# Kernel tuning notes

Measured on AMD Instinct MI355X. Metric: run time of the kernel, lower is better.

## Reference

```python
import jax, jax.numpy as jnp
import numpy as np

# channel indices (consistent with INPUT_CHANNELS=6)
WALL, SRC_REAL, SRC_IMAG, GATE_REAL, GATE_IMAG = 0, 1, 2, 3, 4
READOUT_THRESHOLD = 0.35
EPS = 1e-08


def _neighbor_sum(a):
    # zero-padded 4-neighbor shift-sum over last two dims of [B,1,H,W]
    H, W = a.shape[-2], a.shape[-1]
    p = jnp.pad(a, ((0, 0), (0, 0), (1, 1), (1, 1)))
    return (p[:, :, 0:H, 1:W + 1] + p[:, :, 2:H + 2, 1:W + 1]
            + p[:, :, 1:H + 1, 0:W] + p[:, :, 1:H + 1, 2:W + 2])


def _phase_vectors(phase_classes):
    k = jnp.arange(phase_classes, dtype=jnp.float32)
    th = 2.0 * jnp.pi * k / phase_classes
    return jnp.stack([jnp.cos(th), jnp.sin(th)], axis=1)  # [P,2]


def _fixed_logits(vec, phase_classes):
    phases = _phase_vectors(phase_classes)
    mag2 = jnp.sum(vec ** 2, axis=1)
    none = (READOUT_THRESHOLD * READOUT_THRESHOLD - mag2) * 8.0
    phase_logits = (vec @ phases.T - READOUT_THRESHOLD) * 12.0
    return jnp.concatenate([none[:, None], phase_logits], axis=1)


def setup_inputs() -> dict:
    key = jax.random.key(0)
    k1, k2 = jax.random.split(key)
    x = jax.random.uniform(k1, (32, 6, 256, 256), dtype=jnp.float32)
    target = jax.random.randint(k2, (32, 2), 0, 256, dtype=jnp.int64 if jax.config.jax_enable_x64 else jnp.int32)
    return {"x": x, "target": target, "steps": 24}


def reference(x, target, steps):
    phase_classes = 8
    free = 1.0 - x[:, WALL:WALL + 1]
    gate_r = x[:, GATE_REAL:GATE_REAL + 1]
    gate_i = x[:, GATE_IMAG:GATE_IMAG + 1]
    wallf = (x[:, WALL:WALL + 1] > 0.5).astype(x.dtype)

    real = x[:, SRC_REAL:SRC_REAL + 1] * free
    imag = x[:, SRC_IMAG:SRC_IMAG + 1] * free
    written = (real ** 2 + imag ** 2) > EPS
    state_r, state_i = real, imag

    def step(carry, _):
        real, imag, sr, si, written = carry
        inc_r = _neighbor_sum(real)
        inc_i = _neighbor_sum(imag)
        # FIXED_PRISMION: complex multiply with gate
        nr = inc_r * gate_r - inc_i * gate_i
        ni = inc_r * gate_i + inc_i * gate_r
        pre_wall = jnp.mean(jnp.sqrt(nr * nr + ni * ni) * wallf)
        real = nr * free
        imag = ni * free
        active = ((real ** 2 + imag ** 2) > EPS) & (~written)
        sr = jnp.where(active, real, sr)
        si = jnp.where(active, imag, si)
        written = written | active
        real = jnp.where(active, real, jnp.zeros_like(real))
        imag = jnp.where(active, imag, jnp.zeros_like(imag))
        act = jnp.mean(jnp.abs(real) + jnp.abs(imag))
        return (real, imag, sr, si, written), (pre_wall, act)

    (real, imag, state_r, state_i, written), (pre_walls, acts) = jax.lax.scan(
        step, (real, imag, state_r, state_i, written), None, length=int(steps))

    vec_map = jnp.concatenate([state_r, state_i], axis=1)  # [B,2,H,W]
    wall = x[:, WALL:WALL + 1] > 0.5
    leak = jnp.mean((((jnp.sum(vec_map ** 2, axis=1, keepdims=True) ** 0.5) > 0.5) & wall).astype(x.dtype))
    pre_wall_mean = jnp.mean(pre_walls)
    act_mean = jnp.mean(acts)

    b = jnp.arange(vec_map.shape[0])
    vec = vec_map[b, :, target[:, 0], target[:, 1]]  # [B,2]
    logits = _fixed_logits(vec, phase_classes)
    return logits, leak, pre_wall_mean, act_mean
```

## Files before the change

kernel.cpp:

```cpp
#include <hip/hip_runtime.h>
#include <stdint.h>

#define EPSV 1e-8f
#define HH 256
#define WW 256
#define NB 32
#define STEPS 24
#define PLANE (HH * WW)
#define NCELL (NB * PLANE)
#define NBLK 2048
#define TBLK 512
#define CAP 8192
#define FIXS 68719476736.0


__device__ __forceinline__ float block_fsum(float v, float* sm) {
  #pragma unroll
  for (int o = 32; o; o >>= 1) v += __shfl_down(v, o, 64);
  if ((threadIdx.x & 63) == 0) sm[threadIdx.x >> 6] = v;
  __syncthreads();
  float r = 0.0f;
  if (threadIdx.x == 0) r = ((sm[0] + sm[1]) + sm[2]) + sm[3];
  __syncthreads();
  return r;
}

__device__ __forceinline__ int block_isum(int v, int* sm) {
  #pragma unroll
  for (int o = 32; o; o >>= 1) v += __shfl_down(v, o, 64);
  if ((threadIdx.x & 63) == 0) sm[threadIdx.x >> 6] = v;
  __syncthreads();
  int r = 0;
  if (threadIdx.x == 0) r = sm[0] + sm[1] + sm[2] + sm[3];
  __syncthreads();
  return r;
}

__device__ __forceinline__ int block_any(int v, int* sm) {
  if (threadIdx.x == 0) sm[0] = 0;
  __syncthreads();
  if (v) sm[0] = 1;
  __syncthreads();
  int r = sm[0];
  __syncthreads();
  return r;
}

__global__ __launch_bounds__(128) void zero_kernel(int* __restrict__ ctrl) {
  ctrl[threadIdx.x] = 0;
}

__device__ __forceinline__ float2 init_val(const float* xw, const float* xsr,
                                           const float* xsi, int y, int xc) {
  if (y < 0 || y >= HH || xc < 0 || xc >= WW) return make_float2(0.f, 0.f);
  const int yx = y * WW + xc;
  float fr = 1.0f - xw[yx];
  return make_float2(__fmul_rn(xsr[yx], fr), __fmul_rn(xsi[yx], fr));
}

__global__ __launch_bounds__(256) void fused0_kernel(
    const float* __restrict__ x, const int* __restrict__ target,
    float2* __restrict__ bufB, uint32_t* __restrict__ wrw,
    float* __restrict__ pw_part, float* __restrict__ act_part,
    int* __restrict__ ileak_part, float* __restrict__ vec,
    int* __restrict__ ctrl, int* __restrict__ list, uint32_t* __restrict__ cbm) {
  __shared__ float smf[4];
  __shared__ int smi[4];
  const int tx = threadIdx.x;
  const int blk = blockIdx.x;
  const int b = blk >> 6;
  const int y0 = (blk & 63) << 2;
  const int cbase = b * PLANE;
  const float* xw  = x + (size_t)b * 6 * PLANE;
  const float* xsr = xw + 1 * PLANE;
  const float* xsi = xw + 2 * PLANE;
  const float* xgr = xw + 3 * PLANE;
  const float* xgi = xw + 4 * PLANE;
  const int t0 = target[b * 2], t1 = target[b * 2 + 1];

  if (tx < 32) cbm[blk * 32 + tx] = 0;

  float pw = 0.0f, act = 0.0f;
  int leak = 0, any_act = 0;

  float2 rm = init_val(xw, xsr, xsi, y0 - 1, tx);
  float wallc = xw[y0 * WW + tx];
  float2 rc;
  {
    float fr = 1.0f - wallc;
    rc = make_float2(__fmul_rn(xsr[y0 * WW + tx], fr), __fmul_rn(xsi[y0 * WW + tx], fr));
  }

  #pragma unroll
  for (int k = 0; k < 4; ++k) {
    const int y = y0 + k, yx = y * WW + tx;
    float wallp = 0.0f;
    float2 rp = make_float2(0.f, 0.f);
    if (y + 1 < HH) {
      wallp = xw[yx + WW];
      float fr = 1.0f - wallp;
      rp = make_float2(__fmul_rn(xsr[yx + WW], fr), __fmul_rn(xsi[yx + WW], fr));
    }
    float2 lf = init_val(xw, xsr, xsi, y, tx - 1);
    float2 rg = init_val(xw, xsr, xsi, y, tx + 1);

    float inc_r = (rm.x + rp.x) + (lf.x + rg.x);
    float inc_i = (rm.y + rp.y) + (lf.y + rg.y);
    float gr = xgr[yx], gi = xgi[yx];
    float fr = 1.0f - wallc;

    float nr = inc_r * gr - inc_i * gi;
    float ni = inc_r * gi + inc_i * gr;
    if (wallc > 0.5f) pw += sqrtf(nr * nr + ni * ni);

    float r = __fmul_rn(nr, fr);
    float i = __fmul_rn(ni, fr);
    float mag0 = __fadd_rn(__fmul_rn(r, r), __fmul_rn(i, i));
    float magI = __fadd_rn(__fmul_rn(rc.x, rc.x), __fmul_rn(rc.y, rc.y));
    bool writtenI = magI > EPSV;
    bool active = (mag0 > EPSV) && !writtenI;

    if (magI > 0.25f && wallc > 0.5f) ++leak;
    if (active && mag0 > 0.25f && wallc > 0.5f) ++leak;

    float outr = active ? r : 0.0f;
    float outi = active ? i : 0.0f;
    bufB[cbase + yx] = make_float2(outr, outi);
    act += fabsf(outr) + fabsf(outi);
    if (active) any_act = 1;

    if (y == t0 && tx == t1) {
      vec[2 * b] = active ? r : rc.x;
      vec[2 * b + 1] = active ? i : rc.y;
    }

    unsigned long long bw = __ballot(writtenI || active);
    if ((tx & 63) == 0) {
      uint2 v; v.x = (uint32_t)bw; v.y = (uint32_t)(bw >> 32);
      *(uint2*)&wrw[(cbase + yx) >> 5] = v;
    }

    unsigned long long ba = __ballot(active);
    if (ba) {
      const int lane = tx & 63;
      const int ldr = __ffsll((unsigned long long)ba) - 1;
      unsigned lbase = 0;
      if (lane == ldr)
        lbase = atomicAdd((unsigned*)&ctrl[51], (unsigned)__popcll(ba));
      lbase = (unsigned)__shfl((int)lbase, ldr, 64);
      if (active) {
        unsigned pos = lbase + (unsigned)__popcll(ba & ((1ull << lane) - 1ull));
        if (pos < CAP) list[pos] = cbase + yx;
      }
    }
    rm = rc; rc = rp; wallc = wallp;
  }

  float pws = block_fsum(pw, smf);
  float acs = block_fsum(act, smf);
  int lks = block_isum(leak, smi);
  if (tx == 0) { pw_part[blk] = pws; act_part[blk] = acs; ileak_part[blk] = lks; }
  if (block_any(any_act, smi) && tx == 0) ctrl[1] = 1;
}

__global__ __launch_bounds__(512) void sparse1_kernel(
    const float* __restrict__ x, const int* __restrict__ target,
    const float2* __restrict__ bufB, float2* __restrict__ bufA,
    uint32_t* __restrict__ wrw, const int* __restrict__ list,
    uint32_t* __restrict__ cbm, int* __restrict__ ctrl,
    float* __restrict__ vec) {
  __shared__ long long smp[512];
  const int t = threadIdx.x;
  const int gsz = gridDim.x * 512;
  const int n0 = ctrl[51];
  if (n0 > CAP) {
    if (blockIdx.x == 0 && t == 0) ctrl[50] = 1;
    return;
  }
  if (n0 == 0) return;

  long long pwf = 0, actf = 0;
  int leak = 0;

  for (int idx = blockIdx.x * 512 + t; idx < 5 * n0; idx += gsz) {
    const int i = idx / 5, d = idx - 5 * i;
    int cell = list[i];
    int yx = cell & 0xFFFF;
    int y = yx >> 8, xx = yx & 255;
    if (d == 1) { if (y == 0) continue;      cell -= WW; y -= 1; }
    else if (d == 2) { if (y == HH - 1) continue; cell += WW; y += 1; }
    else if (d == 3) { if (xx == 0) continue;     cell -= 1;  xx -= 1; }
    else if (d == 4) { if (xx == WW - 1) continue; cell += 1; xx += 1; }
    const uint32_t bit = 1u << (cell & 31);
    if (atomicOr(&cbm[cell >> 5], bit) & bit) continue;

    const int b = cell >> 16;
    yx = cell & 0xFFFF;
    const float* xw = x + (size_t)b * 6 * PLANE;
    float2 up = (y > 0)       ? bufB[cell - WW] : make_float2(0.f, 0.f);
    float2 dn = (y < HH - 1)  ? bufB[cell + WW] : make_float2(0.f, 0.f);
    float2 lf = (xx > 0)      ? bufB[cell - 1]  : make_float2(0.f, 0.f);
    float2 rg = (xx < WW - 1) ? bufB[cell + 1]  : make_float2(0.f, 0.f);
    float inc_r = (up.x + dn.x) + (lf.x + rg.x);
    float inc_i = (up.y + dn.y) + (lf.y + rg.y);
    float gr = xw[3 * PLANE + yx], gi = xw[4 * PLANE + yx];
    float wall = xw[yx];
    float fr = 1.0f - wall;
    float nr = inc_r * gr - inc_i * gi;
    float ni = inc_r * gi + inc_i * gr;
    if (wall > 0.5f) pwf += (long long)((double)sqrtf(nr * nr + ni * ni) * FIXS);
    float r = __fmul_rn(nr, fr);
    float i2 = __fmul_rn(ni, fr);
    float mag = __fadd_rn(__fmul_rn(r, r), __fmul_rn(i2, i2));
    bool wr = (wrw[cell >> 5] >> (cell & 31)) & 1u;
    bool active = (mag > EPSV) && !wr;
    float outr = active ? r : 0.0f;
    float outi = active ? i2 : 0.0f;
    bufA[cell] = make_float2(outr, outi);
    actf += (long long)((double)(fabsf(outr) + fabsf(outi)) * FIXS);
    if (active) {
      atomicOr(&wrw[cell >> 5], bit);
      ctrl[2] = 1;
      if (mag > 0.25f && wall > 0.5f) ++leak;
      if (y == target[b * 2] && xx == target[b * 2 + 1]) {
        vec[2 * b] = r; vec[2 * b + 1] = i2;
      }
    }
  }

  smp[t] = pwf; __syncthreads();
  for (int o = 256; o; o >>= 1) { if (t < o) smp[t] += smp[t + o]; __syncthreads(); }
  if (t == 0 && smp[0]) atomicAdd((unsigned long long*)&ctrl[56], (unsigned long long)smp[0]);
  __syncthreads();
  smp[t] = actf; __syncthreads();
  for (int o = 256; o; o >>= 1) { if (t < o) smp[t] += smp[t + o]; __syncthreads(); }
  if (t == 0 && smp[0]) atomicAdd((unsigned long long*)&ctrl[58], (unsigned long long)smp[0]);
  __syncthreads();
  smp[t] = leak; __syncthreads();
  for (int o = 256; o; o >>= 1) { if (t < o) smp[t] += smp[t + o]; __syncthreads(); }
  if (t == 0 && smp[0]) atomicAdd(&ctrl[52], (int)smp[0]);
}

__device__ __forceinline__ void grid_barrier(int* bar) {
  __syncthreads();
  if (threadIdx.x == 0) {
    __threadfence();
    __hip_atomic_fetch_add(bar, 1, __ATOMIC_RELEASE, __HIP_MEMORY_SCOPE_AGENT);
    int guard = 0;
    while (__hip_atomic_load(bar, __ATOMIC_ACQUIRE, __HIP_MEMORY_SCOPE_AGENT) < TBLK) {
      if (++guard > (1 << 22)) break;
    }
  }
  __syncthreads();
}

__global__ __launch_bounds__(256, 2) void tail_kernel(
    const float* __restrict__ x, const int* __restrict__ target,
    float2* __restrict__ bufA, float2* __restrict__ bufB,
    const uint32_t* __restrict__ wrw, const uint32_t* __restrict__ cbm,
    float* __restrict__ pw_part, float* __restrict__ act_part,
    int* __restrict__ ileak_part, float* __restrict__ vec,
    int* __restrict__ ctrl) {
  int* cnt = ctrl;
  int* bar = ctrl + 25;
  const int ov = ctrl[50];
  const int sstart = ov ? 1 : 2;
  if (cnt[sstart] == 0) return;
  __shared__ float smf[4];
  __shared__ int smi[4];
  const int tx = threadIdx.x;
  const int blk = blockIdx.x;
  const int b = blk >> 4;
  const int y0 = (blk & 15) << 4;
  const int cbase = b * PLANE;
  const float* xw  = x + (size_t)b * 6 * PLANE;
  const float* xgr = xw + 3 * PLANE;
  const float* xgi = xw + 4 * PLANE;
  const int t0 = target[b * 2], t1 = target[b * 2 + 1];

  float wallr[16];
  unsigned wrmask = 0;
  #pragma unroll
  for (int k = 0; k < 16; ++k) {
    const int yx = (y0 + k) * WW + tx;
    wallr[k] = xw[yx];
    if ((wrw[(cbase + yx) >> 5] >> (tx & 31)) & 1u) wrmask |= (1u << k);
  }

  if (!ov) {
    #pragma unroll
    for (int k = 0; k < 16; ++k) {
      const int c = cbase + (y0 + k) * WW + tx;
      if (!((cbm[c >> 5] >> (c & 31)) & 1u)) bufA[c] = make_float2(0.f, 0.f);
    }
    grid_barrier(&bar[0]);
  }

  const float2* cur0 = ov ? (const float2*)bufB : (const float2*)bufA;
  float2* nxt0 = ov ? bufA : bufB;

  for (int s = sstart; s < STEPS; ++s) {
    if (__hip_atomic_load(&cnt[s], __ATOMIC_RELAXED, __HIP_MEMORY_SCOPE_AGENT) == 0) break;
    const int p = (s - sstart) & 1;
    const float2* __restrict__ cur = p ? (const float2*)nxt0 : cur0;
    float2* __restrict__ nxt = p ? (float2*)cur0 : nxt0;

    float pw = 0.0f, act = 0.0f;
    int leak_s = 0, any_act = 0;

    float2 rowm = (y0 > 0) ? cur[cbase + (y0 - 1) * WW + tx] : make_float2(0.f, 0.f);
    float2 rowc = cur[cbase + y0 * WW + tx];

    #pragma unroll
    for (int k = 0; k < 16; ++k) {
      const int y = y0 + k, yx = y * WW + tx;
      float2 rowp = (y < HH - 1) ? cur[cbase + yx + WW] : make_float2(0.f, 0.f);
      float2 lft  = (tx > 0)      ? cur[cbase + yx - 1] : make_float2(0.f, 0.f);
      float2 rgt  = (tx < WW - 1) ? cur[cbase + yx + 1] : make_float2(0.f, 0.f);

      float inc_r = (rowm.x + rowp.x) + (lft.x + rgt.x);
      float inc_i = (rowm.y + rowp.y) + (lft.y + rgt.y);
      float gr = xgr[yx], gi = xgi[yx];
      float wall = wallr[k];
      float fr = 1.0f - wall;

      float nr = inc_r * gr - inc_i * gi;
      float ni = inc_r * gi + inc_i * gr;
      if (wall > 0.5f) pw += sqrtf(nr * nr + ni * ni);

      float r = __fmul_rn(nr, fr);
      float i = __fmul_rn(ni, fr);
      float mag = __fadd_rn(__fmul_rn(r, r), __fmul_rn(i, i));
      bool active = (mag > EPSV) && !((wrmask >> k) & 1u);

      float outr = active ? r : 0.0f;
      float outi = active ? i : 0.0f;
      nxt[cbase + yx] = make_float2(outr, outi);
      act += fabsf(outr) + fabsf(outi);

      if (active) {
        wrmask |= (1u << k);
        any_act = 1;
        if (mag > 0.25f && wall > 0.5f) ++leak_s;
        if (y == t0 && tx == t1) { vec[2 * b] = r; vec[2 * b + 1] = i; }
      }
      rowm = rowc; rowc = rowp;
    }

    float pws = block_fsum(pw, smf);
    float acs = block_fsum(act, smf);
    int lks = block_isum(leak_s, smi);
    if (tx == 0) {
      pw_part[s * NBLK + blk] = pws;
      act_part[s * NBLK + blk] = acs;
      ileak_part[s * NBLK + blk] = lks;
    }
    if (block_any(any_act, smi) && tx == 0)
      __hip_atomic_store(&cnt[s + 1], 1, __ATOMIC_RELAXED, __HIP_MEMORY_SCOPE_AGENT);
    grid_barrier(&bar[s]);
  }
}

__global__ __launch_bounds__(256) void final_kernel(
    const float* __restrict__ pw_part, const float* __restrict__ act_part,
    const int* __restrict__ ileak_part, const int* __restrict__ ctrl,
    const float* __restrict__ vec, float* __restrict__ out) {
  __shared__ double sm[256];
  const int t = threadIdx.x;
  const int* cnt = ctrl;
  const int ov = ctrl[50];

  double pw = 0.0, ac = 0.0, lk = 0.0;
  for (int j = t; j < NBLK; j += 256) {
    pw += (double)pw_part[j];
    ac += (double)act_part[j];
    lk += (double)ileak_part[j];
  }
  for (int s = ov ? 1 : 2; s < STEPS; ++s) {
    if (cnt[s] == 0) break;
    for (int j = t; j < TBLK; j += 256) {
      pw += (double)pw_part[s * NBLK + j];
      ac += (double)act_part[s * NBLK + j];
      lk += (double)ileak_part[s * NBLK + j];
    }
  }
  sm[t] = pw; __syncthreads();
  for (int o = 128; o; o >>= 1) { if (t < o) sm[t] += sm[t + o]; __syncthreads(); }
  double pws = sm[0]; __syncthreads();
  sm[t] = ac; __syncthreads();
  for (int o = 128; o; o >>= 1) { if (t < o) sm[t] += sm[t + o]; __syncthreads(); }
  double acs = sm[0]; __syncthreads();
  sm[t] = lk; __syncthreads();
  for (int o = 128; o; o >>= 1) { if (t < o) sm[t] += sm[t + o]; __syncthreads(); }
  double lks = sm[0];

  pws += (double)((const long long*)ctrl)[28] / FIXS;
  acs += (double)((const long long*)ctrl)[29] / FIXS;
  lks += (double)ctrl[52];

  if (t < NB) {
    float vr = vec[t * 2], vi = vec[t * 2 + 1];
    float mag2 = __fadd_rn(__fmul_rn(vr, vr), __fmul_rn(vi, vi));
    out[t * 9] = (0.35f * 0.35f - mag2) * 8.0f;
    #pragma unroll
    for (int k = 0; k < 8; ++k) {
      float th = (float)(6.283185307179586 * (double)k) / 8.0f;
      float pl = (vr * cosf(th) + vi * sinf(th) - 0.35f) * 12.0f;
      out[t * 9 + 1 + k] = pl;
    }
  }
  if (t == 0) {
    out[288] = (float)(lks / (double)NCELL);
    out[289] = (float)(pws / ((double)STEPS * (double)NCELL));
    out[290] = (float)(acs / ((double)STEPS * (double)NCELL));
  }
}

extern "C" void kernel_launch(void* const* d_in, const int* in_sizes, int n_in,
                              void* d_out, int out_size, void* d_ws, size_t ws_size,
                              hipStream_t stream) {
  const float* x = (const float*)d_in[0];
  const int* target = (const int*)d_in[1];

  char* ws = (char*)d_ws;
  float2* bufA = (float2*)ws;
  float2* bufB = bufA + NCELL;
  float* pw_part  = (float*)(bufB + NCELL);
  float* act_part = pw_part + STEPS * NBLK;
  int* ileak_part = (int*)(act_part + STEPS * NBLK);
  float* vec      = (float*)(ileak_part + STEPS * NBLK);
  uint32_t* wrw   = (uint32_t*)(vec + 2 * NB);
  uint32_t* cbm   = wrw + NCELL / 32;
  int* list       = (int*)(cbm + NCELL / 32);
  int* ctrl       = list + CAP;

  zero_kernel<<<1, 128, 0, stream>>>(ctrl);
  fused0_kernel<<<NBLK, 256, 0, stream>>>(x, target, bufB, wrw,
                                          pw_part, act_part, ileak_part, vec,
                                          ctrl, list, cbm);
  sparse1_kernel<<<16, 512, 0, stream>>>(x, target, bufB, bufA, wrw, list, cbm,
                                         ctrl, vec);
  tail_kernel<<<TBLK, 256, 0, stream>>>(x, target, bufA, bufB, wrw, cbm,
                                        pw_part, act_part, ileak_part, vec, ctrl);
  final_kernel<<<1, 256, 0, stream>>>(pw_part, act_part, ileak_part, ctrl, vec,
                                      (float*)d_out);
}
```

Measured before the change: 38.59 us.

## Fuse sparse step, tail loop and final reduction into one persistent kernel

Merges the sparse second-step kernel, the persistent tail stepping kernel and the single-block final reduction into one cooperative mega kernel separated by grid barriers. Step-0 partial sums are pre-reduced by 24 spare blocks before the first barrier, and block 0 produces the outputs at the end. This removes two kernel launches and their gaps. In exchange it adds an extra grid barrier, stronger fences in the barrier, and spreads the sparse work over 512 blocks of 256 threads instead of 16 blocks of 512.

```diff
diff --git a/kernel.cpp b/kernel.cpp
--- a/kernel.cpp
+++ b/kernel.cpp
@@ -163,253 +163,248 @@
   if (block_any(any_act, smi) && tx == 0) ctrl[1] = 1;
 }
 
-__global__ __launch_bounds__(512) void sparse1_kernel(
-    const float* __restrict__ x, const int* __restrict__ target,
-    const float2* __restrict__ bufB, float2* __restrict__ bufA,
-    uint32_t* __restrict__ wrw, const int* __restrict__ list,
-    uint32_t* __restrict__ cbm, int* __restrict__ ctrl,
-    float* __restrict__ vec) {
-  __shared__ long long smp[512];
-  const int t = threadIdx.x;
-  const int gsz = gridDim.x * 512;
-  const int n0 = ctrl[51];
-  if (n0 > CAP) {
-    if (blockIdx.x == 0 && t == 0) ctrl[50] = 1;
-    return;
-  }
-  if (n0 == 0) return;
-
-  long long pwf = 0, actf = 0;
-  int leak = 0;
-
-  for (int idx = blockIdx.x * 512 + t; idx < 5 * n0; idx += gsz) {
-    const int i = idx / 5, d = idx - 5 * i;
-    int cell = list[i];
-    int yx = cell & 0xFFFF;
-    int y = yx >> 8, xx = yx & 255;
-    if (d == 1) { if (y == 0) continue;      cell -= WW; y -= 1; }
-    else if (d == 2) { if (y == HH - 1) continue; cell += WW; y += 1; }
-    else if (d == 3) { if (xx == 0) continue;     cell -= 1;  xx -= 1; }
-    else if (d == 4) { if (xx == WW - 1) continue; cell += 1; xx += 1; }
-    const uint32_t bit = 1u << (cell & 31);
-    if (atomicOr(&cbm[cell >> 5], bit) & bit) continue;
-
-    const int b = cell >> 16;
-    yx = cell & 0xFFFF;
-    const float* xw = x + (size_t)b * 6 * PLANE;
-    float2 up = (y > 0)       ? bufB[cell - WW] : make_float2(0.f, 0.f);
-    float2 dn = (y < HH - 1)  ? bufB[cell + WW] : make_float2(0.f, 0.f);
-    float2 lf = (xx > 0)      ? bufB[cell - 1]  : make_float2(0.f, 0.f);
-    float2 rg = (xx < WW - 1) ? bufB[cell + 1]  : make_float2(0.f, 0.f);
-    float inc_r = (up.x + dn.x) + (lf.x + rg.x);
-    float inc_i = (up.y + dn.y) + (lf.y + rg.y);
-    float gr = xw[3 * PLANE + yx], gi = xw[4 * PLANE + yx];
-    float wall = xw[yx];
-    float fr = 1.0f - wall;
-    float nr = inc_r * gr - inc_i * gi;
-    float ni = inc_r * gi + inc_i * gr;
-    if (wall > 0.5f) pwf += (long long)((double)sqrtf(nr * nr + ni * ni) * FIXS);
-    float r = __fmul_rn(nr, fr);
-    float i2 = __fmul_rn(ni, fr);
-    float mag = __fadd_rn(__fmul_rn(r, r), __fmul_rn(i2, i2));
-    bool wr = (wrw[cell >> 5] >> (cell & 31)) & 1u;
-    bool active = (mag > EPSV) && !wr;
-    float outr = active ? r : 0.0f;
-    float outi = active ? i2 : 0.0f;
-    bufA[cell] = make_float2(outr, outi);
-    actf += (long long)((double)(fabsf(outr) + fabsf(outi)) * FIXS);
-    if (active) {
-      atomicOr(&wrw[cell >> 5], bit);
-      ctrl[2] = 1;
-      if (mag > 0.25f && wall > 0.5f) ++leak;
-      if (y == target[b * 2] && xx == target[b * 2 + 1]) {
-        vec[2 * b] = r; vec[2 * b + 1] = i2;
-      }
-    }
-  }
-
-  smp[t] = pwf; __syncthreads();
-  for (int o = 256; o; o >>= 1) { if (t < o) smp[t] += smp[t + o]; __syncthreads(); }
-  if (t == 0 && smp[0]) atomicAdd((unsigned long long*)&ctrl[56], (unsigned long long)smp[0]);
-  __syncthreads();
-  smp[t] = actf; __syncthreads();
-  for (int o = 256; o; o >>= 1) { if (t < o) smp[t] += smp[t + o]; __syncthreads(); }
-  if (t == 0 && smp[0]) atomicAdd((unsigned long long*)&ctrl[58], (unsigned long long)smp[0]);
-  __syncthreads();
-  smp[t] = leak; __syncthreads();
-  for (int o = 256; o; o >>= 1) { if (t < o) smp[t] += smp[t + o]; __syncthreads(); }
-  if (t == 0 && smp[0]) atomicAdd(&ctrl[52], (int)smp[0]);
-}
-
 __device__ __forceinline__ void grid_barrier(int* bar) {
   __syncthreads();
+  __threadfence();
   if (threadIdx.x == 0) {
-    __threadfence();
-    __hip_atomic_fetch_add(bar, 1, __ATOMIC_RELEASE, __HIP_MEMORY_SCOPE_AGENT);
+    __hip_atomic_fetch_add(bar, 1, __ATOMIC_ACQ_REL, __HIP_MEMORY_SCOPE_AGENT);
     int guard = 0;
     while (__hip_atomic_load(bar, __ATOMIC_ACQUIRE, __HIP_MEMORY_SCOPE_AGENT) < TBLK) {
       if (++guard > (1 << 22)) break;
     }
   }
   __syncthreads();
-}
-
-__global__ __launch_bounds__(256, 2) void tail_kernel(
+  __threadfence();
+}
+
+__global__ __launch_bounds__(256, 2) void mega_kernel(
     const float* __restrict__ x, const int* __restrict__ target,
     float2* __restrict__ bufA, float2* __restrict__ bufB,
-    const uint32_t* __restrict__ wrw, const uint32_t* __restrict__ cbm,
+    uint32_t* __restrict__ wrw, uint32_t* __restrict__ cbm,
+    const int* __restrict__ list,
     float* __restrict__ pw_part, float* __restrict__ act_part,
-    int* __restrict__ ileak_part, float* __restrict__ vec,
-    int* __restrict__ ctrl) {
-  int* cnt = ctrl;
-  int* bar = ctrl + 25;
-  const int ov = ctrl[50];
-  const int sstart = ov ? 1 : 2;
-  if (cnt[sstart] == 0) return;
+    int* __restrict__ ileak_part, float* __restrict__ red,
+    float* __restrict__ vec, int* __restrict__ ctrl, float* __restrict__ out) {
+  __shared__ long long smp[256];
+  __shared__ double smd[256];
   __shared__ float smf[4];
   __shared__ int smi[4];
   const int tx = threadIdx.x;
   const int blk = blockIdx.x;
-  const int b = blk >> 4;
-  const int y0 = (blk & 15) << 4;
-  const int cbase = b * PLANE;
-  const float* xw  = x + (size_t)b * 6 * PLANE;
-  const float* xgr = xw + 3 * PLANE;
-  const float* xgi = xw + 4 * PLANE;
-  const int t0 = target[b * 2], t1 = target[b * 2 + 1];
-
-  float wallr[16];
-  unsigned wrmask = 0;
-  #pragma unroll
-  for (int k = 0; k < 16; ++k) {
-    const int yx = (y0 + k) * WW + tx;
-    wallr[k] = xw[yx];
-    if ((wrw[(cbase + yx) >> 5] >> (tx & 31)) & 1u) wrmask |= (1u << k);
-  }
-
+  int* cnt = ctrl;
+  int* bar = ctrl + 25;
+  const int n0 = ctrl[51];
+  const bool ov = (n0 > CAP);
+
+  long long pwf = 0, actf = 0;
+  int leak = 0;
   if (!ov) {
+    for (int idx = blk * 256 + tx; idx < 5 * n0; idx += TBLK * 256) {
+      const int i = idx / 5, d = idx - 5 * i;
+      int cell = list[i];
+      int yx = cell & 0xFFFF;
+      int y = yx >> 8, xx = yx & 255;
+      if (d == 1) { if (y == 0) continue;       cell -= WW; y -= 1; }
+      else if (d == 2) { if (y == HH - 1) continue;  cell += WW; y += 1; }
+      else if (d == 3) { if (xx == 0) continue;      cell -= 1;  xx -= 1; }
+      else if (d == 4) { if (xx == WW - 1) continue; cell += 1;  xx += 1; }
+      const uint32_t bit = 1u << (cell & 31);
+      if (atomicOr(&cbm[cell >> 5], bit) & bit) continue;
+
+      const int bb = cell >> 16;
+      yx = cell & 0xFFFF;
+      const float* xwb = x + (size_t)bb * 6 * PLANE;
+      float2 up = (y > 0)       ? bufB[cell - WW] : make_float2(0.f, 0.f);
+      float2 dn = (y < HH - 1)  ? bufB[cell + WW] : make_float2(0.f, 0.f);
+      float2 lf = (xx > 0)      ? bufB[cell - 1]  : make_float2(0.f, 0.f);
+      float2 rg = (xx < WW - 1) ? bufB[cell + 1]  : make_float2(0.f, 0.f);
+      float inc_r = (up.x + dn.x) + (lf.x + rg.x);
+      float inc_i = (up.y + dn.y) + (lf.y + rg.y);
+      float gr = xwb[3 * PLANE + yx], gi = xwb[4 * PLANE + yx];
+      float wall = xwb[yx];
+      float fr = 1.0f - wall;
+      float nr = inc_r * gr - inc_i * gi;
+      float ni = inc_r * gi + inc_i * gr;
+      if (wall > 0.5f) pwf += (long long)((double)sqrtf(nr * nr + ni * ni) * FIXS);
+      float r = __fmul_rn(nr, fr);
+      float i2 = __fmul_rn(ni, fr);
+      float mag = __fadd_rn(__fmul_rn(r, r), __fmul_rn(i2, i2));
+      bool wr = (wrw[cell >> 5] >> (cell & 31)) & 1u;
+      bool active = (mag > EPSV) && !wr;
+      float outr = active ? r : 0.0f;
+      float outi = active ? i2 : 0.0f;
+      bufA[cell] = make_float2(outr, outi);
+      actf += (long long)((double)(fabsf(outr) + fabsf(outi)) * FIXS);
+      if (active) {
+        atomicOr(&wrw[cell >> 5], bit);
+        cnt[2] = 1;
+        if (mag > 0.25f && wall > 0.5f) ++leak;
+        if (y == target[bb * 2] && xx == target[bb * 2 + 1]) {
+          vec[2 * bb] = r; vec[2 * bb + 1] = i2;
+        }
+      }
+    }
+  }
+  smp[tx] = pwf; __syncthreads();
+  for (int o = 128; o; o >>= 1) { if (tx < o) smp[tx] += smp[tx + o]; __syncthreads(); }
+  if (tx == 0 && smp[0]) atomicAdd((unsigned long long*)&ctrl[56], (unsigned long long)smp[0]);
+  __syncthreads();
+  smp[tx] = actf; __syncthreads();
+  for (int o = 128; o; o >>= 1) { if (tx < o) smp[tx] += smp[tx + o]; __syncthreads(); }
+  if (tx == 0 && smp[0]) atomicAdd((unsigned long long*)&ctrl[58], (unsigned long long)smp[0]);
+  __syncthreads();
+  smp[tx] = leak; __syncthreads();
+  for (int o = 128; o; o >>= 1) { if (tx < o) smp[tx] += smp[tx + o]; __syncthreads(); }
+  if (tx == 0 && smp[0]) atomicAdd(&ctrl[52], (int)smp[0]);
+
+  if (blk >= TBLK - 24) {
+    const int g = blk - (TBLK - 24);
+    const int arr = g >> 3, chunk = g & 7;
+    const int j = chunk * 256 + tx;
+    if (arr == 2) {
+      int s = block_isum(ileak_part[j], smi);
+      if (tx == 0) red[g] = (float)s;
+    } else {
+      float s = block_fsum(arr == 0 ? pw_part[j] : act_part[j], smf);
+      if (tx == 0) red[g] = s;
+    }
+  }
+
+  grid_barrier(&bar[24]);
+
+  const int sstart = ov ? 1 : 2;
+  if (cnt[sstart] != 0) {
+    const int b = blk >> 4;
+    const int y0 = (blk & 15) << 4;
+    const int cbase = b * PLANE;
+    const float* xw  = x + (size_t)b * 6 * PLANE;
+    const float* xgr = xw + 3 * PLANE;
+    const float* xgi = xw + 4 * PLANE;
+    const int t0 = target[b * 2], t1 = target[b * 2 + 1];
+
+    float wallr[16];
+    unsigned wrmask = 0;
     #pragma unroll
     for (int k = 0; k < 16; ++k) {
-      const int c = cbase + (y0 + k) * WW + tx;
-      if (!((cbm[c >> 5] >> (c & 31)) & 1u)) bufA[c] = make_float2(0.f, 0.f);
-    }
-    grid_barrier(&bar[0]);
-  }
-
-  const float2* cur0 = ov ? (const float2*)bufB : (const float2*)bufA;
-  float2* nxt0 = ov ? bufA : bufB;
-
+      const int yx = (y0 + k) * WW + tx;
+      wallr[k] = xw[yx];
+      if ((wrw[(cbase + yx) >> 5] >> (tx & 31)) & 1u) wrmask |= (1u << k);
+    }
+
+    if (!ov) {
+      #pragma unroll
+      for (int k = 0; k < 16; ++k) {
+        const int c = cbase + (y0 + k) * WW + tx;
+        if (!((cbm[c >> 5] >> (c & 31)) & 1u)) bufA[c] = make_float2(0.f, 0.f);
+      }
+      grid_barrier(&bar[0]);
+    }
+
+    const float2* cur0 = ov ? (const float2*)bufB : (const float2*)bufA;
+    float2* nxt0 = ov ? bufA : bufB;
+
+    for (int s = sstart; s < STEPS; ++s) {
+      if (__hip_atomic_load(&cnt[s], __ATOMIC_RELAXED, __HIP_MEMORY_SCOPE_AGENT) == 0) break;
+      const int p = (s - sstart) & 1;
+      const float2* __restrict__ cur = p ? (const float2*)nxt0 : cur0;
+      float2* __restrict__ nxt = p ? (float2*)cur0 : nxt0;
+
+      float pw = 0.0f, act = 0.0f;
+      int leak_s = 0, any_act = 0;
+
+      float2 rowm = (y0 > 0) ? cur[cbase + (y0 - 1) * WW + tx] : make_float2(0.f, 0.f);
+      float2 rowc = cur[cbase + y0 * WW + tx];
+
+      #pragma unroll
+      for (int k = 0; k < 16; ++k) {
+        const int y = y0 + k, yx = y * WW + tx;
+        float2 rowp = (y < HH - 1) ? cur[cbase + yx + WW] : make_float2(0.f, 0.f);
+        float2 lft  = (tx > 0)      ? cur[cbase + yx - 1] : make_float2(0.f, 0.f);
+        float2 rgt  = (tx < WW - 1) ? cur[cbase + yx + 1] : make_float2(0.f, 0.f);
+
+        float inc_r = (rowm.x + rowp.x) + (lft.x + rgt.x);
+        float inc_i = (rowm.y + rowp.y) + (lft.y + rgt.y);
+        float gr = xgr[yx], gi = xgi[yx];
+        float wall = wallr[k];
+        float fr = 1.0f - wall;
+
+        float nr = inc_r * gr - inc_i * gi;
+        float ni = inc_r * gi + inc_i * gr;
+        if (wall > 0.5f) pw += sqrtf(nr * nr + ni * ni);
+
+        float r = __fmul_rn(nr, fr);
+        float i = __fmul_rn(ni, fr);
+        float mag = __fadd_rn(__fmul_rn(r, r), __fmul_rn(i, i));
+        bool active = (mag > EPSV) && !((wrmask >> k) & 1u);
+
+        float outr = active ? r : 0.0f;
+        float outi = active ? i : 0.0f;
+        nxt[cbase + yx] = make_float2(outr, outi);
+        act += fabsf(outr) + fabsf(outi);
+
+        if (active) {
+          wrmask |= (1u << k);
+          any_act = 1;
+          if (mag > 0.25f && wall > 0.5f) ++leak_s;
+          if (y == t0 && tx == t1) { vec[2 * b] = r; vec[2 * b + 1] = i; }
+        }
+        rowm = rowc; rowc = rowp;
+      }
+
+      float pws = block_fsum(pw, smf);
+      float acs = block_fsum(act, smf);
+      int lks = block_isum(leak_s, smi);
+      if (tx == 0) {
+        pw_part[s * NBLK + blk] = pws;
+        act_part[s * NBLK + blk] = acs;
+        ileak_part[s * NBLK + blk] = lks;
+      }
+      if (block_any(any_act, smi) && tx == 0)
+        __hip_atomic_store(&cnt[s + 1], 1, __ATOMIC_RELAXED, __HIP_MEMORY_SCOPE_AGENT);
+      grid_barrier(&bar[s]);
+    }
+  }
+
+  if (blk != 0) return;
+
+  double pw = 0.0, ac = 0.0, lk = 0.0;
   for (int s = sstart; s < STEPS; ++s) {
-    if (__hip_atomic_load(&cnt[s], __ATOMIC_RELAXED, __HIP_MEMORY_SCOPE_AGENT) == 0) break;
-    const int p = (s - sstart) & 1;
-    const float2* __restrict__ cur = p ? (const float2*)nxt0 : cur0;
-    float2* __restrict__ nxt = p ? (float2*)cur0 : nxt0;
-
-    float pw = 0.0f, act = 0.0f;
-    int leak_s = 0, any_act = 0;
-
-    float2 rowm = (y0 > 0) ? cur[cbase + (y0 - 1) * WW + tx] : make_float2(0.f, 0.f);
-    float2 rowc = cur[cbase + y0 * WW + tx];
-
-    #pragma unroll
-    for (int k = 0; k < 16; ++k) {
-      const int y = y0 + k, yx = y * WW + tx;
-      float2 rowp = (y < HH - 1) ? cur[cbase + yx + WW] : make_float2(0.f, 0.f);
-      float2 lft  = (tx > 0)      ? cur[cbase + yx - 1] : make_float2(0.f, 0.f);
-      float2 rgt  = (tx < WW - 1) ? cur[cbase + yx + 1] : make_float2(0.f, 0.f);
-
-      float inc_r = (rowm.x + rowp.x) + (lft.x + rgt.x);
-      float inc_i = (rowm.y + rowp.y) + (lft.y + rgt.y);
-      float gr = xgr[yx], gi = xgi[yx];
-      float wall = wallr[k];
-      float fr = 1.0f - wall;
-
-      float nr = inc_r * gr - inc_i * gi;
-      float ni = inc_r * gi + inc_i * gr;
-      if (wall > 0.5f) pw += sqrtf(nr * nr + ni * ni);
-
-      float r = __fmul_rn(nr, fr);
-      float i = __fmul_rn(ni, fr);
-      float mag = __fadd_rn(__fmul_rn(r, r), __fmul_rn(i, i));
-      bool active = (mag > EPSV) && !((wrmask >> k) & 1u);
-
-      float outr = active ? r : 0.0f;
-      float outi = active ? i : 0.0f;
-      nxt[cbase + yx] = make_float2(outr, outi);
-      act += fabsf(outr) + fabsf(outi);
-
-      if (active) {
-        wrmask |= (1u << k);
-        any_act = 1;
-        if (mag > 0.25f && wall > 0.5f) ++leak_s;
-        if (y == t0 && tx == t1) { vec[2 * b] = r; vec[2 * b + 1] = i; }
-      }
-      rowm = rowc; rowc = rowp;
-    }
-
-    float pws = block_fsum(pw, smf);
-    float acs = block_fsum(act, smf);
-    int lks = block_isum(leak_s, smi);
-    if (tx == 0) {
-      pw_part[s * NBLK + blk] = pws;
-      act_part[s * NBLK + blk] = acs;
-      ileak_part[s * NBLK + blk] = lks;
-    }
-    if (block_any(any_act, smi) && tx == 0)
-      __hip_atomic_store(&cnt[s + 1], 1, __ATOMIC_RELAXED, __HIP_MEMORY_SCOPE_AGENT);
-    grid_barrier(&bar[s]);
-  }
-}
-
-__global__ __launch_bounds__(256) void final_kernel(
-    const float* __restrict__ pw_part, const float* __restrict__ act_part,
-    const int* __restrict__ ileak_part, const int* __restrict__ ctrl,
-    const float* __restrict__ vec, float* __restrict__ out) {
-  __shared__ double sm[256];
-  const int t = threadIdx.x;
-  const int* cnt = ctrl;
-  const int ov = ctrl[50];
-
-  double pw = 0.0, ac = 0.0, lk = 0.0;
-  for (int j = t; j < NBLK; j += 256) {
-    pw += (double)pw_part[j];
-    ac += (double)act_part[j];
-    lk += (double)ileak_part[j];
-  }
-  for (int s = ov ? 1 : 2; s < STEPS; ++s) {
     if (cnt[s] == 0) break;
-    for (int j = t; j < TBLK; j += 256) {
-      pw += (double)pw_part[s * NBLK + j];
-      ac += (double)act_part[s * NBLK + j];
-      lk += (double)ileak_part[s * NBLK + j];
-    }
-  }
-  sm[t] = pw; __syncthreads();
-  for (int o = 128; o; o >>= 1) { if (t < o) sm[t] += sm[t + o]; __syncthreads(); }
-  double pws = sm[0]; __syncthreads();
-  sm[t] = ac; __syncthreads();
-  for (int o = 128; o; o >>= 1) { if (t < o) sm[t] += sm[t + o]; __syncthreads(); }
-  double acs = sm[0]; __syncthreads();
-  sm[t] = lk; __syncthreads();
-  for (int o = 128; o; o >>= 1) { if (t < o) sm[t] += sm[t + o]; __syncthreads(); }
-  double lks = sm[0];
-
-  pws += (double)((const long long*)ctrl)[28] / FIXS;
-  acs += (double)((const long long*)ctrl)[29] / FIXS;
-  lks += (double)ctrl[52];
-
-  if (t < NB) {
-    float vr = vec[t * 2], vi = vec[t * 2 + 1];
+    pw += (double)pw_part[s * NBLK + tx] + (double)pw_part[s * NBLK + tx + 256];
+    ac += (double)act_part[s * NBLK + tx] + (double)act_part[s * NBLK + tx + 256];
+    lk += (double)ileak_part[s * NBLK + tx] + (double)ileak_part[s * NBLK + tx + 256];
+  }
+  smd[tx] = pw; __syncthreads();
+  for (int o = 128; o; o >>= 1) { if (tx < o) smd[tx] += smd[tx + o]; __syncthreads(); }
+  double pws = smd[0]; __syncthreads();
+  smd[tx] = ac; __syncthreads();
+  for (int o = 128; o; o >>= 1) { if (tx < o) smd[tx] += smd[tx + o]; __syncthreads(); }
+  double acs = smd[0]; __syncthreads();
+  smd[tx] = lk; __syncthreads();
+  for (int o = 128; o; o >>= 1) { if (tx < o) smd[tx] += smd[tx + o]; __syncthreads(); }
+  double lks = smd[0];
+
+  if (tx < NB) {
+    float vr = vec[tx * 2], vi = vec[tx * 2 + 1];
     float mag2 = __fadd_rn(__fmul_rn(vr, vr), __fmul_rn(vi, vi));
-    out[t * 9] = (0.35f * 0.35f - mag2) * 8.0f;
+    out[tx * 9] = (0.35f * 0.35f - mag2) * 8.0f;
     #pragma unroll
     for (int k = 0; k < 8; ++k) {
       float th = (float)(6.283185307179586 * (double)k) / 8.0f;
       float pl = (vr * cosf(th) + vi * sinf(th) - 0.35f) * 12.0f;
-      out[t * 9 + 1 + k] = pl;
-    }
-  }
-  if (t == 0) {
+      out[tx * 9 + 1 + k] = pl;
+    }
+  }
+  if (tx == 0) {
+    #pragma unroll
+    for (int g = 0; g < 8; ++g) {
+      pws += (double)red[g];
+      acs += (double)red[8 + g];
+      lks += (double)red[16 + g];
+    }
+    pws += (double)((const long long*)ctrl)[28] / FIXS;
+    acs += (double)((const long long*)ctrl)[29] / FIXS;
+    lks += (double)ctrl[52];
     out[288] = (float)(lks / (double)NCELL);
     out[289] = (float)(pws / ((double)STEPS * (double)NCELL));
     out[290] = (float)(acs / ((double)STEPS * (double)NCELL));
@@ -433,15 +428,13 @@
   uint32_t* cbm   = wrw + NCELL / 32;
   int* list       = (int*)(cbm + NCELL / 32);
   int* ctrl       = list + CAP;
+  float* red      = (float*)(ctrl + 128);
 
   zero_kernel<<<1, 128, 0, stream>>>(ctrl);
   fused0_kernel<<<NBLK, 256, 0, stream>>>(x, target, bufB, wrw,
                                           pw_part, act_part, ileak_part, vec,
                                           ctrl, list, cbm);
-  sparse1_kernel<<<16, 512, 0, stream>>>(x, target, bufB, bufA, wrw, list, cbm,
-                                         ctrl, vec);
-  tail_kernel<<<TBLK, 256, 0, stream>>>(x, target, bufA, bufB, wrw, cbm,
-                                        pw_part, act_part, ileak_part, vec, ctrl);
-  final_kernel<<<1, 256, 0, stream>>>(pw_part, act_part, ileak_part, ctrl, vec,
-                                      (float*)d_out);
-}
+  mega_kernel<<<TBLK, 256, 0, stream>>>(x, target, bufA, bufB, wrw, cbm, list,
+                                        pw_part, act_part, ileak_part, red,
+                                        vec, ctrl, (float*)d_out);
+}
```

New measurement: 102.8 us. 2.66x slower.

## Fold final reduction into sparse and tail kernels, dropping separate final launch

Applied to the files above, without the earlier changes.

Removes the standalone final_kernel launch. The last-finishing sparse1 block (elected via an atomic ticket counter) computes the outputs when propagation has already died. Otherwise block 0 of the persistent tail kernel does the final reduction after its last grid barrier. This saves one kernel launch and its dependency gap, at the cost of more control logic and an extra ticket counter in ctrl that must be zeroed beforehand.

```diff
diff --git a/kernel.cpp b/kernel.cpp
--- a/kernel.cpp
+++ b/kernel.cpp
@@ -10,6 +10,7 @@
 #define NCELL (NB * PLANE)
 #define NBLK 2048
 #define TBLK 512
+#define SBLK 16
 #define CAP 8192
 #define FIXS 68719476736.0
 
@@ -168,35 +169,34 @@
     const float2* __restrict__ bufB, float2* __restrict__ bufA,
     uint32_t* __restrict__ wrw, const int* __restrict__ list,
     uint32_t* __restrict__ cbm, int* __restrict__ ctrl,
-    float* __restrict__ vec) {
+    float* __restrict__ vec,
+    const float* __restrict__ pw_part, const float* __restrict__ act_part,
+    const int* __restrict__ ileak_part, float* __restrict__ out) {
   __shared__ long long smp[512];
+  __shared__ double smd[512];
+  __shared__ int swin;
   const int t = threadIdx.x;
-  const int gsz = gridDim.x * 512;
   const int n0 = ctrl[51];
-  if (n0 > CAP) {
-    if (blockIdx.x == 0 && t == 0) ctrl[50] = 1;
-    return;
-  }
-  if (n0 == 0) return;
+  if (n0 > CAP) return;
 
   long long pwf = 0, actf = 0;
   int leak = 0;
 
-  for (int idx = blockIdx.x * 512 + t; idx < 5 * n0; idx += gsz) {
+  for (int idx = blockIdx.x * 512 + t; idx < 5 * n0; idx += SBLK * 512) {
     const int i = idx / 5, d = idx - 5 * i;
     int cell = list[i];
     int yx = cell & 0xFFFF;
     int y = yx >> 8, xx = yx & 255;
-    if (d == 1) { if (y == 0) continue;      cell -= WW; y -= 1; }
-    else if (d == 2) { if (y == HH - 1) continue; cell += WW; y += 1; }
-    else if (d == 3) { if (xx == 0) continue;     cell -= 1;  xx -= 1; }
-    else if (d == 4) { if (xx == WW - 1) continue; cell += 1; xx += 1; }
+    if (d == 1) { if (y == 0) continue;       cell -= WW; y -= 1; }
+    else if (d == 2) { if (y == HH - 1) continue;  cell += WW; y += 1; }
+    else if (d == 3) { if (xx == 0) continue;      cell -= 1;  xx -= 1; }
+    else if (d == 4) { if (xx == WW - 1) continue; cell += 1;  xx += 1; }
     const uint32_t bit = 1u << (cell & 31);
     if (atomicOr(&cbm[cell >> 5], bit) & bit) continue;
 
-    const int b = cell >> 16;
+    const int bb = cell >> 16;
     yx = cell & 0xFFFF;
-    const float* xw = x + (size_t)b * 6 * PLANE;
+    const float* xw = x + (size_t)bb * 6 * PLANE;
     float2 up = (y > 0)       ? bufB[cell - WW] : make_float2(0.f, 0.f);
     float2 dn = (y < HH - 1)  ? bufB[cell + WW] : make_float2(0.f, 0.f);
     float2 lf = (xx > 0)      ? bufB[cell - 1]  : make_float2(0.f, 0.f);
@@ -220,10 +220,10 @@
     actf += (long long)((double)(fabsf(outr) + fabsf(outi)) * FIXS);
     if (active) {
       atomicOr(&wrw[cell >> 5], bit);
-      ctrl[2] = 1;
+      __hip_atomic_store(&ctrl[2], 1, __ATOMIC_RELAXED, __HIP_MEMORY_SCOPE_AGENT);
       if (mag > 0.25f && wall > 0.5f) ++leak;
-      if (y == target[b * 2] && xx == target[b * 2 + 1]) {
-        vec[2 * b] = r; vec[2 * b + 1] = i2;
+      if (y == target[bb * 2] && xx == target[bb * 2 + 1]) {
+        vec[2 * bb] = r; vec[2 * bb + 1] = i2;
       }
     }
   }
@@ -239,164 +239,34 @@
   smp[t] = leak; __syncthreads();
   for (int o = 256; o; o >>= 1) { if (t < o) smp[t] += smp[t + o]; __syncthreads(); }
   if (t == 0 && smp[0]) atomicAdd(&ctrl[52], (int)smp[0]);
-}
-
-__device__ __forceinline__ void grid_barrier(int* bar) {
-  __syncthreads();
-  if (threadIdx.x == 0) {
+
+  __syncthreads();
+  if (t == 0) {
     __threadfence();
-    __hip_atomic_fetch_add(bar, 1, __ATOMIC_RELEASE, __HIP_MEMORY_SCOPE_AGENT);
-    int guard = 0;
-    while (__hip_atomic_load(bar, __ATOMIC_ACQUIRE, __HIP_MEMORY_SCOPE_AGENT) < TBLK) {
-      if (++guard > (1 << 22)) break;
-    }
-  }
-  __syncthreads();
-}
-
-__global__ __launch_bounds__(256, 2) void tail_kernel(
-    const float* __restrict__ x, const int* __restrict__ target,
-    float2* __restrict__ bufA, float2* __restrict__ bufB,
-    const uint32_t* __restrict__ wrw, const uint32_t* __restrict__ cbm,
-    float* __restrict__ pw_part, float* __restrict__ act_part,
-    int* __restrict__ ileak_part, float* __restrict__ vec,
-    int* __restrict__ ctrl) {
-  int* cnt = ctrl;
-  int* bar = ctrl + 25;
-  const int ov = ctrl[50];
-  const int sstart = ov ? 1 : 2;
-  if (cnt[sstart] == 0) return;
-  __shared__ float smf[4];
-  __shared__ int smi[4];
-  const int tx = threadIdx.x;
-  const int blk = blockIdx.x;
-  const int b = blk >> 4;
-  const int y0 = (blk & 15) << 4;
-  const int cbase = b * PLANE;
-  const float* xw  = x + (size_t)b * 6 * PLANE;
-  const float* xgr = xw + 3 * PLANE;
-  const float* xgi = xw + 4 * PLANE;
-  const int t0 = target[b * 2], t1 = target[b * 2 + 1];
-
-  float wallr[16];
-  unsigned wrmask = 0;
-  #pragma unroll
-  for (int k = 0; k < 16; ++k) {
-    const int yx = (y0 + k) * WW + tx;
-    wallr[k] = xw[yx];
-    if ((wrw[(cbase + yx) >> 5] >> (tx & 31)) & 1u) wrmask |= (1u << k);
-  }
-
-  if (!ov) {
-    #pragma unroll
-    for (int k = 0; k < 16; ++k) {
-      const int c = cbase + (y0 + k) * WW + tx;
-      if (!((cbm[c >> 5] >> (c & 31)) & 1u)) bufA[c] = make_float2(0.f, 0.f);
-    }
-    grid_barrier(&bar[0]);
-  }
-
-  const float2* cur0 = ov ? (const float2*)bufB : (const float2*)bufA;
-  float2* nxt0 = ov ? bufA : bufB;
-
-  for (int s = sstart; s < STEPS; ++s) {
-    if (__hip_atomic_load(&cnt[s], __ATOMIC_RELAXED, __HIP_MEMORY_SCOPE_AGENT) == 0) break;
-    const int p = (s - sstart) & 1;
-    const float2* __restrict__ cur = p ? (const float2*)nxt0 : cur0;
-    float2* __restrict__ nxt = p ? (float2*)cur0 : nxt0;
-
-    float pw = 0.0f, act = 0.0f;
-    int leak_s = 0, any_act = 0;
-
-    float2 rowm = (y0 > 0) ? cur[cbase + (y0 - 1) * WW + tx] : make_float2(0.f, 0.f);
-    float2 rowc = cur[cbase + y0 * WW + tx];
-
-    #pragma unroll
-    for (int k = 0; k < 16; ++k) {
-      const int y = y0 + k, yx = y * WW + tx;
-      float2 rowp = (y < HH - 1) ? cur[cbase + yx + WW] : make_float2(0.f, 0.f);
-      float2 lft  = (tx > 0)      ? cur[cbase + yx - 1] : make_float2(0.f, 0.f);
-      float2 rgt  = (tx < WW - 1) ? cur[cbase + yx + 1] : make_float2(0.f, 0.f);
-
-      float inc_r = (rowm.x + rowp.x) + (lft.x + rgt.x);
-      float inc_i = (rowm.y + rowp.y) + (lft.y + rgt.y);
-      float gr = xgr[yx], gi = xgi[yx];
-      float wall = wallr[k];
-      float fr = 1.0f - wall;
-
-      float nr = inc_r * gr - inc_i * gi;
-      float ni = inc_r * gi + inc_i * gr;
-      if (wall > 0.5f) pw += sqrtf(nr * nr + ni * ni);
-
-      float r = __fmul_rn(nr, fr);
-      float i = __fmul_rn(ni, fr);
-      float mag = __fadd_rn(__fmul_rn(r, r), __fmul_rn(i, i));
-      bool active = (mag > EPSV) && !((wrmask >> k) & 1u);
-
-      float outr = active ? r : 0.0f;
-      float outi = active ? i : 0.0f;
-      nxt[cbase + yx] = make_float2(outr, outi);
-      act += fabsf(outr) + fabsf(outi);
-
-      if (active) {
-        wrmask |= (1u << k);
-        any_act = 1;
-        if (mag > 0.25f && wall > 0.5f) ++leak_s;
-        if (y == t0 && tx == t1) { vec[2 * b] = r; vec[2 * b + 1] = i; }
-      }
-      rowm = rowc; rowc = rowp;
-    }
-
-    float pws = block_fsum(pw, smf);
-    float acs = block_fsum(act, smf);
-    int lks = block_isum(leak_s, smi);
-    if (tx == 0) {
-      pw_part[s * NBLK + blk] = pws;
-      act_part[s * NBLK + blk] = acs;
-      ileak_part[s * NBLK + blk] = lks;
-    }
-    if (block_any(any_act, smi) && tx == 0)
-      __hip_atomic_store(&cnt[s + 1], 1, __ATOMIC_RELAXED, __HIP_MEMORY_SCOPE_AGENT);
-    grid_barrier(&bar[s]);
-  }
-}
-
-__global__ __launch_bounds__(256) void final_kernel(
-    const float* __restrict__ pw_part, const float* __restrict__ act_part,
-    const int* __restrict__ ileak_part, const int* __restrict__ ctrl,
-    const float* __restrict__ vec, float* __restrict__ out) {
-  __shared__ double sm[256];
-  const int t = threadIdx.x;
-  const int* cnt = ctrl;
-  const int ov = ctrl[50];
+    int old = __hip_atomic_fetch_add(&ctrl[60], 1, __ATOMIC_ACQ_REL,
+                                     __HIP_MEMORY_SCOPE_AGENT);
+    swin = (old == SBLK - 1) ? 1 : 0;
+  }
+  __syncthreads();
+  if (!swin) return;
+  if (__hip_atomic_load(&ctrl[2], __ATOMIC_RELAXED, __HIP_MEMORY_SCOPE_AGENT) != 0)
+    return;
 
   double pw = 0.0, ac = 0.0, lk = 0.0;
-  for (int j = t; j < NBLK; j += 256) {
+  for (int j = t; j < NBLK; j += 512) {
     pw += (double)pw_part[j];
     ac += (double)act_part[j];
     lk += (double)ileak_part[j];
   }
-  for (int s = ov ? 1 : 2; s < STEPS; ++s) {
-    if (cnt[s] == 0) break;
-    for (int j = t; j < TBLK; j += 256) {
-      pw += (double)pw_part[s * NBLK + j];
-      ac += (double)act_part[s * NBLK + j];
-      lk += (double)ileak_part[s * NBLK + j];
-    }
-  }
-  sm[t] = pw; __syncthreads();
-  for (int o = 128; o; o >>= 1) { if (t < o) sm[t] += sm[t + o]; __syncthreads(); }
-  double pws = sm[0]; __syncthreads();
-  sm[t] = ac; __syncthreads();
-  for (int o = 128; o; o >>= 1) { if (t < o) sm[t] += sm[t + o]; __syncthreads(); }
-  double acs = sm[0]; __syncthreads();
-  sm[t] = lk; __syncthreads();
-  for (int o = 128; o; o >>= 1) { if (t < o) sm[t] += sm[t + o]; __syncthreads(); }
-  double lks = sm[0];
-
-  pws += (double)((const long long*)ctrl)[28] / FIXS;
-  acs += (double)((const long long*)ctrl)[29] / FIXS;
-  lks += (double)ctrl[52];
+  smd[t] = pw; __syncthreads();
+  for (int o = 256; o; o >>= 1) { if (t < o) smd[t] += smd[t + o]; __syncthreads(); }
+  double pws = smd[0]; __syncthreads();
+  smd[t] = ac; __syncthreads();
+  for (int o = 256; o; o >>= 1) { if (t < o) smd[t] += smd[t + o]; __syncthreads(); }
+  double acs = smd[0]; __syncthreads();
+  smd[t] = lk; __syncthreads();
+  for (int o = 256; o; o >>= 1) { if (t < o) smd[t] += smd[t + o]; __syncthreads(); }
+  double lks = smd[0];
 
   if (t < NB) {
     float vr = vec[t * 2], vi = vec[t * 2 + 1];
@@ -410,6 +280,180 @@
     }
   }
   if (t == 0) {
+    pws += (double)((const long long*)ctrl)[28] / FIXS;
+    acs += (double)((const long long*)ctrl)[29] / FIXS;
+    lks += (double)ctrl[52];
+    out[288] = (float)(lks / (double)NCELL);
+    out[289] = (float)(pws / ((double)STEPS * (double)NCELL));
+    out[290] = (float)(acs / ((double)STEPS * (double)NCELL));
+  }
+}
+
+__device__ __forceinline__ void grid_barrier(int* bar) {
+  __syncthreads();
+  if (threadIdx.x == 0) {
+    __threadfence();
+    __hip_atomic_fetch_add(bar, 1, __ATOMIC_RELEASE, __HIP_MEMORY_SCOPE_AGENT);
+    int guard = 0;
+    while (__hip_atomic_load(bar, __ATOMIC_ACQUIRE, __HIP_MEMORY_SCOPE_AGENT) < TBLK) {
+      if (++guard > (1 << 22)) break;
+    }
+  }
+  __syncthreads();
+}
+
+__global__ __launch_bounds__(256, 2) void tailfinal_kernel(
+    const float* __restrict__ x, const int* __restrict__ target,
+    float2* __restrict__ bufA, float2* __restrict__ bufB,
+    const uint32_t* __restrict__ wrw, const uint32_t* __restrict__ cbm,
+    float* __restrict__ pw_part, float* __restrict__ act_part,
+    int* __restrict__ ileak_part, float* __restrict__ vec,
+    int* __restrict__ ctrl, float* __restrict__ out) {
+  __shared__ double smd[256];
+  __shared__ float smf[4];
+  __shared__ int smi[4];
+  const int tx = threadIdx.x;
+  const int blk = blockIdx.x;
+  int* cnt = ctrl;
+  int* bar = ctrl + 25;
+  const int n0 = ctrl[51];
+  const bool ov = (n0 > CAP);
+  const int sstart = ov ? 1 : 2;
+  if (!ov && cnt[2] == 0) return;
+
+  if (cnt[sstart] != 0) {
+    const int b = blk >> 4;
+    const int y0 = (blk & 15) << 4;
+    const int cbase = b * PLANE;
+    const float* xw  = x + (size_t)b * 6 * PLANE;
+    const float* xgr = xw + 3 * PLANE;
+    const float* xgi = xw + 4 * PLANE;
+    const int t0 = target[b * 2], t1 = target[b * 2 + 1];
+
+    float wallr[16];
+    unsigned wrmask = 0;
+    #pragma unroll
+    for (int k = 0; k < 16; ++k) {
+      const int c = cbase + (y0 + k) * WW + tx;
+      wallr[k] = xw[(y0 + k) * WW + tx];
+      if ((wrw[c >> 5] >> (c & 31)) & 1u) wrmask |= (1u << k);
+    }
+
+    if (!ov) {
+      #pragma unroll
+      for (int k = 0; k < 16; ++k) {
+        const int c = cbase + (y0 + k) * WW + tx;
+        if (!((cbm[c >> 5] >> (c & 31)) & 1u)) bufA[c] = make_float2(0.f, 0.f);
+      }
+      grid_barrier(&bar[0]);
+    }
+
+    const float2* cur0 = ov ? (const float2*)bufB : (const float2*)bufA;
+    float2* nxt0 = ov ? bufA : bufB;
+
+    for (int s = sstart; s < STEPS; ++s) {
+      if (__hip_atomic_load(&cnt[s], __ATOMIC_RELAXED, __HIP_MEMORY_SCOPE_AGENT) == 0) break;
+      const int p = (s - sstart) & 1;
+      const float2* __restrict__ cur = p ? (const float2*)nxt0 : cur0;
+      float2* __restrict__ nxt = p ? (float2*)cur0 : nxt0;
+
+      float pw = 0.0f, act = 0.0f;
+      int leak_s = 0, any_act = 0;
+
+      float2 rowm = (y0 > 0) ? cur[cbase + (y0 - 1) * WW + tx] : make_float2(0.f, 0.f);
+      float2 rowc = cur[cbase + y0 * WW + tx];
+
+      #pragma unroll
+      for (int k = 0; k < 16; ++k) {
+        const int y = y0 + k, yx = y * WW + tx;
+        float2 rowp = (y < HH - 1) ? cur[cbase + yx + WW] : make_float2(0.f, 0.f);
+        float2 lft  = (tx > 0)      ? cur[cbase + yx - 1] : make_float2(0.f, 0.f);
+        float2 rgt  = (tx < WW - 1) ? cur[cbase + yx + 1] : make_float2(0.f, 0.f);
+
+        float inc_r = (rowm.x + rowp.x) + (lft.x + rgt.x);
+        float inc_i = (rowm.y + rowp.y) + (lft.y + rgt.y);
+        float gr = xgr[yx], gi = xgi[yx];
+        float wall = wallr[k];
+        float fr = 1.0f - wall;
+
+        float nr = inc_r * gr - inc_i * gi;
+        float ni = inc_r * gi + inc_i * gr;
+        if (wall > 0.5f) pw += sqrtf(nr * nr + ni * ni);
+
+        float r = __fmul_rn(nr, fr);
+        float i = __fmul_rn(ni, fr);
+        float mag = __fadd_rn(__fmul_rn(r, r), __fmul_rn(i, i));
+        bool active = (mag > EPSV) && !((wrmask >> k) & 1u);
+
+        float outr = active ? r : 0.0f;
+        float outi = active ? i : 0.0f;
+        nxt[cbase + yx] = make_float2(outr, outi);
+        act += fabsf(outr) + fabsf(outi);
+
+        if (active) {
+          wrmask |= (1u << k);
+          any_act = 1;
+          if (mag > 0.25f && wall > 0.5f) ++leak_s;
+          if (y == t0 && tx == t1) { vec[2 * b] = r; vec[2 * b + 1] = i; }
+        }
+        rowm = rowc; rowc = rowp;
+      }
+
+      float pws = block_fsum(pw, smf);
+      float acs = block_fsum(act, smf);
+      int lks = block_isum(leak_s, smi);
+      if (tx == 0) {
+        pw_part[s * NBLK + blk] = pws;
+        act_part[s * NBLK + blk] = acs;
+        ileak_part[s * NBLK + blk] = lks;
+      }
+      if (block_any(any_act, smi) && tx == 0)
+        __hip_atomic_store(&cnt[s + 1], 1, __ATOMIC_RELAXED, __HIP_MEMORY_SCOPE_AGENT);
+      grid_barrier(&bar[s]);
+    }
+  }
+
+  if (blk != 0) return;
+
+  double pw = 0.0, ac = 0.0, lk = 0.0;
+  for (int j = tx; j < NBLK; j += 256) {
+    pw += (double)pw_part[j];
+    ac += (double)act_part[j];
+    lk += (double)ileak_part[j];
+  }
+  for (int s = sstart; s < STEPS; ++s) {
+    if (cnt[s] == 0) break;
+    for (int j = tx; j < TBLK; j += 256) {
+      pw += (double)pw_part[s * NBLK + j];
+      ac += (double)act_part[s * NBLK + j];
+      lk += (double)ileak_part[s * NBLK + j];
+    }
+  }
+  smd[tx] = pw; __syncthreads();
+  for (int o = 128; o; o >>= 1) { if (tx < o) smd[tx] += smd[tx + o]; __syncthreads(); }
+  double pws = smd[0]; __syncthreads();
+  smd[tx] = ac; __syncthreads();
+  for (int o = 128; o; o >>= 1) { if (tx < o) smd[tx] += smd[tx + o]; __syncthreads(); }
+  double acs = smd[0]; __syncthreads();
+  smd[tx] = lk; __syncthreads();
+  for (int o = 128; o; o >>= 1) { if (tx < o) smd[tx] += smd[tx + o]; __syncthreads(); }
+  double lks = smd[0];
+
+  if (tx < NB) {
+    float vr = vec[tx * 2], vi = vec[tx * 2 + 1];
+    float mag2 = __fadd_rn(__fmul_rn(vr, vr), __fmul_rn(vi, vi));
+    out[tx * 9] = (0.35f * 0.35f - mag2) * 8.0f;
+    #pragma unroll
+    for (int k = 0; k < 8; ++k) {
+      float th = (float)(6.283185307179586 * (double)k) / 8.0f;
+      float pl = (vr * cosf(th) + vi * sinf(th) - 0.35f) * 12.0f;
+      out[tx * 9 + 1 + k] = pl;
+    }
+  }
+  if (tx == 0) {
+    pws += (double)((const long long*)ctrl)[28] / FIXS;
+    acs += (double)((const long long*)ctrl)[29] / FIXS;
+    lks += (double)ctrl[52];
     out[288] = (float)(lks / (double)NCELL);
     out[289] = (float)(pws / ((double)STEPS * (double)NCELL));
     out[290] = (float)(acs / ((double)STEPS * (double)NCELL));
@@ -438,10 +482,11 @@
   fused0_kernel<<<NBLK, 256, 0, stream>>>(x, target, bufB, wrw,
                                           pw_part, act_part, ileak_part, vec,
                                           ctrl, list, cbm);
-  sparse1_kernel<<<16, 512, 0, stream>>>(x, target, bufB, bufA, wrw, list, cbm,
-                                         ctrl, vec);
-  tail_kernel<<<TBLK, 256, 0, stream>>>(x, target, bufA, bufB, wrw, cbm,
-                                        pw_part, act_part, ileak_part, vec, ctrl);
-  final_kernel<<<1, 256, 0, stream>>>(pw_part, act_part, ileak_part, ctrl, vec,
-                                      (float*)d_out);
-}
+  sparse1_kernel<<<SBLK, 512, 0, stream>>>(x, target, bufB, bufA, wrw, list,
+                                           cbm, ctrl, vec,
+                                           pw_part, act_part, ileak_part,
+                                           (float*)d_out);
+  tailfinal_kernel<<<TBLK, 256, 0, stream>>>(x, target, bufA, bufB, wrw, cbm,
+                                             pw_part, act_part, ileak_part,
+                                             vec, ctrl, (float*)d_out);
+}
```

Result: no change. 37.94 us (-1.7%).
